# Kernel optimization log

Measured on AMD Instinct MI355X. Metric: run time of the kernel, lower is better.

Reference implementation:

```python
import jax, jax.numpy as jnp
import numpy as np

B, MAXN, D, H, S = 64, 512, 512, 8, 32
DH = D // H          # per-head dim = 64
N = B * MAXN         # 32768 total nodes
E = 524288           # ~avg degree 16
EPS = 1e-5


def setup_inputs() -> dict:
    key = jax.random.key(0)
    ks = jax.random.split(key, 18)
    s = 0.05
    x_dense = jax.random.normal(ks[0], (B, MAXN, D), jnp.float32)
    x = jax.random.normal(ks[1], (N, D), jnp.float32)
    src = jax.random.randint(ks[2], (E,), 0, N)
    # destinations kept within the same graph as the source
    dst = (src // MAXN) * MAXN + jax.random.randint(ks[3], (E,), 0, MAXN)
    edge_index = jnp.stack([src, dst]).astype(jnp.int32)
    batch = (jnp.arange(N) // MAXN).astype(jnp.int32)  # sorted, 512 nodes/graph
    seed = jax.random.normal(ks[4], (S, 1, D), jnp.float32) * s
    # per-head GCN conv weights concatenated along output dim: [D, H*DH] == [D, D]
    Wk = jax.random.normal(ks[5], (D, D), jnp.float32) * s
    bk = jnp.zeros((D,), jnp.float32)
    Wv = jax.random.normal(ks[6], (D, D), jnp.float32) * s
    bv = jnp.zeros((D,), jnp.float32)
    q_proj_weight = jax.random.normal(ks[7], (D, D), jnp.float32) * s
    Wo = jax.random.normal(ks[8], (D, D), jnp.float32) * s
    bo = jnp.zeros((D,), jnp.float32)
    Wff = jax.random.normal(ks[9], (D, D), jnp.float32) * s
    bff = jnp.zeros((D,), jnp.float32)
    gamma_h = jnp.ones((D,), jnp.float32)
    beta_h = jnp.zeros((D,), jnp.float32)
    gamma_z = jnp.ones((D,), jnp.float32)
    beta_z = jnp.zeros((D,), jnp.float32)
    return dict(x_dense=x_dense, x=x, edge_index=edge_index, batch=batch,
                seed=seed, Wk=Wk, bk=bk, Wv=Wv, bv=bv,
                q_proj_weight=q_proj_weight, Wo=Wo, bo=bo, Wff=Wff, bff=bff,
                gamma_h=gamma_h, beta_h=beta_h, gamma_z=gamma_z, beta_z=beta_z)


def _gcn(x, W, b, src, dst):
    # PyG GCNConv with self-loops + symmetric norm; all H heads fused via W [D, H*DH]
    xw = x @ W                                   # [N, D]
    idx = jnp.arange(N)
    src_f = jnp.concatenate([src, idx])
    dst_f = jnp.concatenate([dst, idx])
    deg = jax.ops.segment_sum(jnp.ones_like(dst_f, dtype=x.dtype), dst_f, num_segments=N)
    dinv = jax.lax.rsqrt(deg)                    # deg >= 1 (self-loops)
    norm = dinv[src_f] * dinv[dst_f]             # [E+N]
    out = jax.ops.segment_sum(xw[src_f] * norm[:, None], dst_f, num_segments=N)
    return out + b


def _to_dense(feat, batch):
    # to_dense_batch for sorted batch vector; padded slots are zeros
    counts = jax.ops.segment_sum(jnp.ones((N,), jnp.int32), batch, num_segments=B)
    start = jnp.cumsum(counts) - counts
    pos = jnp.arange(N) - start[batch]
    return jnp.zeros((B, MAXN, feat.shape[-1]), feat.dtype).at[batch, pos].set(feat)


def _layernorm(x, g, b):
    m = jnp.mean(x, -1, keepdims=True)
    v = jnp.mean(jnp.square(x - m), -1, keepdims=True)
    return (x - m) * jax.lax.rsqrt(v + EPS) * g + b


def reference(x_dense, x, edge_index, batch, seed, Wk, bk, Wv, bv,
              q_proj_weight, Wo, bo, Wff, bff, gamma_h, beta_h, gamma_z, beta_z):
    src, dst = edge_index[0], edge_index[1]
    k_nodes = _gcn(x, Wk, bk, src, dst)          # [N, D] (H heads concat)
    v_nodes = _gcn(x, Wv, bv, src, dst)
    k_dense = _to_dense(k_nodes, batch)          # [B, MAXN, D]
    v_dense = _to_dense(v_nodes, batch)

    # query: seed [S,1,D] repeated over batch -> [S,B,D]; q projection (F.linear)
    query = jnp.broadcast_to(seed, (S, B, D))
    q = jnp.einsum('sbd,ed->sbe', query, q_proj_weight)
    scale = 1.0 / jnp.sqrt(jnp.float32(DH))
    qh = (q * scale).reshape(S, B, H, DH).transpose(1, 2, 0, 3)     # [B,H,S,DH]
    kh = k_dense.reshape(B, MAXN, H, DH).transpose(0, 2, 1, 3)      # [B,H,N,DH]
    vh = v_dense.reshape(B, MAXN, H, DH).transpose(0, 2, 1, 3)
    scores = jnp.einsum('bhsd,bhnd->bhsn', qh, kh)                  # [B,H,S,MAXN]
    attn = jax.nn.softmax(scores, axis=-1)                          # no padding mask (faithful)
    ctx = jnp.einsum('bhsn,bhnd->bhsd', attn, vh)                   # [B,H,S,DH]
    ctx = ctx.transpose(0, 2, 1, 3).reshape(B, S, D)                # heads concat
    attn_out = ctx @ Wo.T + bo                                      # [B,S,D]

    query_bse = jnp.broadcast_to(seed.transpose(1, 0, 2), (B, S, D))
    embed = _layernorm(query_bse + attn_out, gamma_h, beta_h)
    embed = _layernorm(embed + embed @ Wff.T + bff, gamma_z, beta_z)
    return embed
```

## Files before the change

### kernel.cpp

```cpp
#include <hip/hip_runtime.h>
#include <hip/hip_bf16.h>

#define BN   64
#define MAXN 512
#define DIM  512
#define NH   8
#define NS   32
#define NN   32768
#define NE   524288
#define NBLK 256
#define EPB  (NE / NBLK)
#define MP   (2048 * 512)

typedef __hip_bfloat16 bf16;
using bf16x8 = __attribute__((ext_vector_type(8))) short;
using f32x4  = __attribute__((ext_vector_type(4))) float;

__device__ int            g_cnt[NN];
__device__ int            g_off[NN + 1];
__device__ int            g_csr[NE];
__device__ unsigned short g_hist[(long)NBLK * NN];
__device__ unsigned short g_bpfx[(long)NBLK * NN];
__device__ float g_dinv[NN];
__device__ bf16  g_xb[NN * DIM];
__device__ bf16  g_agg[NN * DIM];
__device__ bf16  g_aggT[NN * DIM];
__device__ bf16  g_qf[256 * DIM];
__device__ bf16  g_wob[DIM * DIM];
__device__ bf16  g_wvb[DIM * DIM];
__device__ bf16  g_wvo[DIM * 8 * DIM];
__device__ float g_bvo[DIM];
__device__ bf16  g_wffT[DIM * DIM];
__device__ float g_q[NS * DIM];
__device__ bf16  g_sc[BN * 256 * MAXN];
__device__ bf16  g_cp[BN * NS * 8 * DIM];
__device__ float g_part[4 * MP];
__device__ float g_h1[BN * NS * DIM];
__device__ bf16  g_h1b[BN * NS * DIM];

__device__ inline float bf2f(unsigned short u) {
    union { unsigned int i; float f; } x; x.i = ((unsigned int)u) << 16; return x.f;
}

__device__ inline void gll16(const bf16* g, bf16* l) {
    __builtin_amdgcn_global_load_lds(
        (const __attribute__((address_space(1))) void*)g,
        (__attribute__((address_space(3))) void*)l, 16, 0, 0);
}

__global__ __launch_bounds__(512) void k_histprep(const int* __restrict__ dst,
                                                  const float* __restrict__ seed,
                                                  const float* __restrict__ Wq,
                                                  const float* __restrict__ Wo,
                                                  const float* __restrict__ Wv,
                                                  const float* __restrict__ Wff,
                                                  const float* __restrict__ bo,
                                                  const float* __restrict__ bv) {
    __shared__ unsigned int h[NN];
    int blk = blockIdx.x, tid = threadIdx.x;
    if (blk < NBLK) {
        for (int i = tid; i < NN; i += 512) h[i] = 0;
        __syncthreads();
#pragma unroll
        for (int j = 0; j < EPB / 512; j++) {
            int e = blk * EPB + j * 512 + tid;
            atomicAdd(&h[dst[e]], 1u);
        }
        __syncthreads();
        unsigned short* out = g_hist + (long)blk * NN;
        for (int i = tid; i < NN; i += 512) out[i] = (unsigned short)h[i];
    } else if (blk < 288) {
        int i = (blk - 256) * 512 + tid;
        int s = i >> 9, e = i & 511;
        const float* sr = seed + s * DIM;
        const float* wr = Wq + e * DIM;
        float a0 = 0.f, a1 = 0.f;
        for (int d = 0; d < DIM; d += 8) {
            float4 a = *(const float4*)(sr + d);
            float4 b = *(const float4*)(wr + d);
            float4 c = *(const float4*)(sr + d + 4);
            float4 w = *(const float4*)(wr + d + 4);
            a0 += a.x * b.x + a.y * b.y + a.z * b.z + a.w * b.w;
            a1 += c.x * w.x + c.y * w.y + c.z * w.z + c.w * w.w;
        }
        g_q[i] = (a0 + a1) * 0.125f;
    } else if (blk < 480) {
        long t = (long)(blk - 288) * 512 + tid;
        const float* src; bf16* dstp; long off;
        if (t < 32768)      { src = Wo;  dstp = g_wob;  off = t; }
        else if (t < 65536) { src = Wv;  dstp = g_wvb;  off = t - 32768; }
        else                { src = Wff; dstp = g_wffT; off = t - 65536; }
        long i = off * 8;
        float4 a = *(const float4*)(src + i);
        float4 b = *(const float4*)(src + i + 4);
        float v[8] = {a.x, a.y, a.z, a.w, b.x, b.y, b.z, b.w};
        bf16x8 o;
#pragma unroll
        for (int j = 0; j < 8; j++) { bf16 q = __float2bfloat16(v[j]); o[j] = *(short*)&q; }
        *(bf16x8*)(dstp + i) = o;
    } else {
        int e = tid;
        const float* orow = Wo + (long)e * DIM;
        float a0 = 0.f, a1 = 0.f;
        for (int c = 0; c < DIM; c += 8) {
            float4 a = *(const float4*)(bv + c);
            float4 w = *(const float4*)(orow + c);
            float4 xx = *(const float4*)(bv + c + 4);
            float4 u = *(const float4*)(orow + c + 4);
            a0 += a.x * w.x + a.y * w.y + a.z * w.z + a.w * w.w;
            a1 += xx.x * u.x + xx.y * u.y + xx.z * u.z + xx.w * u.w;
        }
        g_bvo[e] = bo[e] + a0 + a1;
    }
}

__global__ __launch_bounds__(256) void k_colscan() {
    int v = blockIdx.x * 256 + threadIdx.x;
    unsigned int s = 0;
#pragma unroll 8
    for (int p = 0; p < NBLK; p++) {
        unsigned int hh = g_hist[(long)p * NN + v];
        g_bpfx[(long)p * NN + v] = (unsigned short)s;
        s += hh;
    }
    g_cnt[v] = (int)s;
    g_dinv[v] = rsqrtf(1.0f + (float)s);
}

__global__ void k_scan() {
    __shared__ int part[1024];
    int t = threadIdx.x;
    int base = t * 32;
    int loc[32]; int s = 0;
#pragma unroll
    for (int i = 0; i < 32; i++) { loc[i] = g_cnt[base + i]; s += loc[i]; }
    part[t] = s; __syncthreads();
    for (int o = 1; o < 1024; o <<= 1) {
        int v = (t >= o) ? part[t - o] : 0;
        __syncthreads();
        part[t] += v;
        __syncthreads();
    }
    int ex = (t == 0) ? 0 : part[t - 1];
#pragma unroll
    for (int i = 0; i < 32; i++) { g_off[base + i] = ex; ex += loc[i]; }
    if (t == 1023) g_off[NN] = ex;
}

__global__ __launch_bounds__(512) void k_fillxb(const int* __restrict__ src,
                                                const int* __restrict__ dst,
                                                const float* __restrict__ x,
                                                const float* __restrict__ Wk) {
    __shared__ unsigned int l[NN];
    int blk = blockIdx.x, tid = threadIdx.x;
    if (blk < NBLK) {
        const unsigned short* bp = g_bpfx + (long)blk * NN;
        for (int i = tid; i < NN; i += 512) l[i] = bp[i];
        __syncthreads();
#pragma unroll
        for (int j = 0; j < EPB / 512; j++) {
            int e = blk * EPB + j * 512 + tid;
            int v = dst[e];
            unsigned int r = atomicAdd(&l[v], 1u);
            g_csr[g_off[v] + r] = src[e];
        }
    } else if (blk < 4352) {
        long i = (long)(blk - 256) * (512 * 8) + (long)tid * 8;
        int node = (int)(i >> 9);
        float w = g_dinv[node];
        float4 a = *(const float4*)(x + i);
        float4 b = *(const float4*)(x + i + 4);
        float v[8] = {a.x, a.y, a.z, a.w, b.x, b.y, b.z, b.w};
        bf16x8 o;
#pragma unroll
        for (int j = 0; j < 8; j++) { bf16 t = __float2bfloat16(v[j] * w); o[j] = *(short*)&t; }
        *(bf16x8*)(g_xb + i) = o;
    } else {
        int i = (blk - 4352) * 512 + tid;
        int hs = i >> 9, d = i & 511;
        int h = hs >> 5, s = hs & 31;
        const float* qr = g_q + s * DIM + h * 64;
        const float* wr = Wk + d * DIM + h * 64;
        float a0 = 0.f, a1 = 0.f;
        for (int t2 = 0; t2 < 64; t2 += 8) {
            float4 a = *(const float4*)(qr + t2);
            float4 w = *(const float4*)(wr + t2);
            float4 c = *(const float4*)(qr + t2 + 4);
            float4 u = *(const float4*)(wr + t2 + 4);
            a0 += a.x * w.x + a.y * w.y + a.z * w.z + a.w * w.w;
            a1 += c.x * u.x + c.y * u.y + c.z * u.z + c.w * u.w;
        }
        g_qf[i] = __float2bfloat16(a0 + a1);
    }
}

__global__ __launch_bounds__(256) void k_gather2() {
    __shared__ float sA[4][576];
    int bid = blockIdx.x;
    int node = (bid & 7) * 4096 + (bid >> 3);
    int w = threadIdx.x >> 6, lane = threadIdx.x & 63;

    float2 acc[4];
#pragma unroll
    for (int j = 0; j < 4; j++) acc[j] = make_float2(0.f, 0.f);

    auto addrow = [&](int s) {
        int4 d = ((const int4*)(g_xb + (long)s * DIM))[lane];
        union { int i; float f; } lo, hi;
#pragma unroll
        for (int j = 0; j < 4; j++) {
            int dw = (j == 0) ? d.x : (j == 1) ? d.y : (j == 2) ? d.z : d.w;
            lo.i = dw << 16;
            hi.i = dw & 0xffff0000;
            acc[j] += make_float2(lo.f, hi.f);
        }
    };

    if (w == 0) addrow(node);
    int e0 = g_off[node], e1 = g_off[node + 1];
    int deg = e1 - e0;
    int m16 = e0 + ((deg >> 4) << 4);
    for (int eb = e0 + w * 4; eb < m16; eb += 16) {
        int s0 = g_csr[eb], s1 = g_csr[eb + 1], s2 = g_csr[eb + 2], s3 = g_csr[eb + 3];
        addrow(s0); addrow(s1); addrow(s2); addrow(s3);
    }
    for (int e = m16 + w; e < e1; e += 4) addrow(g_csr[e]);

#pragma unroll
    for (int j = 0; j < 4; j++) {
        sA[w][lane * 9 + j * 2]     = acc[j].x;
        sA[w][lane * 9 + j * 2 + 1] = acc[j].y;
    }
    __syncthreads();

    int t = threadIdx.x;
    int idx = (t >> 2) * 9 + 2 * (t & 3);
    float s0 = 0.f, s1 = 0.f;
#pragma unroll
    for (int ww = 0; ww < 4; ww++) { s0 += sA[ww][idx]; s1 += sA[ww][idx + 1]; }
    float dd = g_dinv[node];
    bf16 b0 = __float2bfloat16(s0 * dd), b1 = __float2bfloat16(s1 * dd);
    unsigned int word = (unsigned int)*(unsigned short*)&b0 |
                        ((unsigned int)*(unsigned short*)&b1 << 16);
    ((unsigned int*)(g_agg + (long)node * DIM))[t] = word;
}

__device__ __forceinline__ void gemm128(const bf16* __restrict__ A, long lda,
                                        const bf16* __restrict__ Bt, long ldb,
                                        long row0, long col0, int kbeg, int kend,
                                        bf16 (*As)[128 * 32], bf16 (*Bs)[128 * 32],
                                        f32x4 acc[4][4]) {
    int tid = threadIdx.x;
    int lane = tid & 63, wave = tid >> 6;
    int wr = wave >> 1, wc = wave & 1;
    int fr = lane & 15, fq = lane >> 4;
    int rchunk = (fq ^ ((fr >> 1) & 3)) * 8;
    int u0 = wave * 128 + lane;
    int sr0 = u0 >> 2, sc0 = ((u0 & 3) ^ ((sr0 >> 1) & 3)) * 8;
    int u1 = u0 + 64;
    int sr1 = u1 >> 2, sc1 = ((u1 & 3) ^ ((sr1 >> 1) & 3)) * 8;

    auto stage = [&](int buf, int kt) {
        gll16(A + (row0 + sr0) * lda + kt + sc0, As[buf] + u0 * 8);
        gll16(A + (row0 + sr1) * lda + kt + sc1, As[buf] + u1 * 8);
        gll16(Bt + (col0 + sr0) * ldb + kt + sc0, Bs[buf] + u0 * 8);
        gll16(Bt + (col0 + sr1) * ldb + kt + sc1, Bs[buf] + u1 * 8);
    };

    stage(0, kbeg);
    __syncthreads();
    for (int kt = kbeg; kt < kend; kt += 32) {
        int buf = ((kt - kbeg) >> 5) & 1;
        if (kt + 32 < kend) stage(buf ^ 1, kt + 32);
        bf16x8 af[4], bfv[4];
#pragma unroll
        for (int mi = 0; mi < 4; mi++)
            af[mi] = *(const bf16x8*)(As[buf] + (wr * 64 + mi * 16 + fr) * 32 + rchunk);
#pragma unroll
        for (int ni = 0; ni < 4; ni++)
            bfv[ni] = *(const bf16x8*)(Bs[buf] + (wc * 64 + ni * 16 + fr) * 32 + rchunk);
#pragma unroll
        for (int mi = 0; mi < 4; mi++)
#pragma unroll
            for (int ni = 0; ni < 4; ni++)
                acc[mi][ni] = __builtin_amdgcn_mfma_f32_16x16x32_bf16(af[mi], bfv[ni], acc[mi][ni], 0, 0, 0);
        __syncthreads();
    }
}

#define ACC_INIT                                             \
    f32x4 acc[4][4];                                         \
    _Pragma("unroll")                                        \
    for (int i = 0; i < 4; i++)                              \
        _Pragma("unroll")                                    \
        for (int j = 0; j < 4; j++) acc[i][j] = (f32x4){0.f, 0.f, 0.f, 0.f}; \
    int lane = threadIdx.x & 63, wave = threadIdx.x >> 6;    \
    int wr = wave >> 1, wc = wave & 1;                       \
    int fr = lane & 15, fq = lane >> 4;

__global__ __launch_bounds__(256) void k_aggsc() {
    __shared__ __align__(16) char smem[32768];
    int blk = blockIdx.x;
    if (blk < 512) {
        bf16 (*As)[128 * 32] = (bf16(*)[128 * 32])smem;
        bf16 (*Bs)[128 * 32] = (bf16(*)[128 * 32])(smem + 16384);
        int b = blk & 63, bx = (blk >> 6) & 1, by = blk >> 7;
        ACC_INIT
        long row0 = (long)bx * 128, col0 = (long)by * 128;
        gemm128(g_qf, DIM, g_agg + (long)b * (MAXN * DIM), DIM, row0, col0, 0, DIM, As, Bs, acc);
        bf16* out = g_sc + (long)b * (256 * MAXN);
#pragma unroll
        for (int mi = 0; mi < 4; mi++)
#pragma unroll
            for (int ni = 0; ni < 4; ni++) {
                long col = col0 + wc * 64 + ni * 16 + fr;
#pragma unroll
                for (int r = 0; r < 4; r++) {
                    long row = row0 + wr * 64 + mi * 16 + fq * 4 + r;
                    out[row * MAXN + col] = __float2bfloat16(acc[mi][ni][r]);
                }
            }
    } else if (blk < 4608) {
        unsigned short (*L)[72] = (unsigned short(*)[72])smem;
        int id = blk - 512;
        int b = id >> 6, t = id & 63;
        int n0 = (t & 7) * 64, d0 = (t >> 3) * 64;
        int tid = threadIdx.x;
        const unsigned short* src = (const unsigned short*)g_agg + ((long)b * 512 + n0) * 512 + d0;
#pragma unroll
        for (int p = 0; p < 2; p++) {
            int r = (tid >> 3) + 32 * p, c = (tid & 7) * 8;
            *(int4*)&L[r][c] = *(const int4*)(src + (long)r * 512 + c);
        }
        __syncthreads();
        unsigned short* dst = (unsigned short*)g_aggT + ((long)b * 512 + d0) * 512 + n0;
#pragma unroll
        for (int p = 0; p < 2; p++) {
            int dr = (tid >> 3) + 32 * p, c0 = (tid & 7) * 8;
            unsigned short tmp[8];
#pragma unroll
            for (int j = 0; j < 8; j++) tmp[j] = L[c0 + j][dr];
            *(int4*)(dst + (long)dr * 512 + c0) = *(int4*)tmp;
        }
    } else {
        bf16 (*As)[128 * 32] = (bf16(*)[128 * 32])smem;
        bf16 (*Bs)[128 * 32] = (bf16(*)[128 * 32])(smem + 16384);
        int wi = blk - 4608;
        int bx = wi & 3, by = (wi >> 2) & 3, h = wi >> 4;
        ACC_INIT
        long row0 = (long)bx * 128, col0 = (long)by * 128;
        gemm128(g_wob, DIM, g_wvb, DIM, row0, col0, h * 64, h * 64 + 64, As, Bs, acc);
#pragma unroll
        for (int mi = 0; mi < 4; mi++)
#pragma unroll
            for (int ni = 0; ni < 4; ni++) {
                long col = col0 + wc * 64 + ni * 16 + fr;
#pragma unroll
                for (int r = 0; r < 4; r++) {
                    long row = row0 + wr * 64 + mi * 16 + fq * 4 + r;
                    g_wvo[row * 4096 + h * 512 + col] = __float2bfloat16(acc[mi][ni][r]);
                }
            }
    }
}

__global__ __launch_bounds__(256) void k_soft() {
    int w = threadIdx.x >> 6, lane = threadIdx.x & 63;
    unsigned short* base = (unsigned short*)g_sc + ((long)blockIdx.x * 16 + w * 4) * MAXN;
#pragma unroll
    for (int r = 0; r < 4; r++) {
        unsigned short* row = base + (long)r * MAXN;
        float v[8]; float m = -1e30f;
#pragma unroll
        for (int k = 0; k < 8; k++) { v[k] = bf2f(row[lane + 64 * k]); m = fmaxf(m, v[k]); }
#pragma unroll
        for (int o = 32; o > 0; o >>= 1) m = fmaxf(m, __shfl_xor(m, o));
        float sum = 0.f;
#pragma unroll
        for (int k = 0; k < 8; k++) { v[k] = __expf(v[k] - m); sum += v[k]; }
#pragma unroll
        for (int o = 32; o > 0; o >>= 1) sum += __shfl_xor(sum, o);
        float inv = 1.0f / sum;
#pragma unroll
        for (int k = 0; k < 8; k++) {
            bf16 t = __float2bfloat16(v[k] * inv);
            row[lane + 64 * k] = *(unsigned short*)&t;
        }
    }
}

__global__ __launch_bounds__(256) void k_pvg() {
    __shared__ bf16 As[2][128 * 32];
    __shared__ bf16 Bs[2][128 * 32];
    int blk = blockIdx.x;
    int b = blk & 63, bx = (blk >> 6) & 1, by = (blk >> 7) & 1, dh = blk >> 8;
    ACC_INIT
    long row0 = (long)bx * 128, col0 = (long)by * 128;
    gemm128(g_sc + (long)b * (256 * MAXN), MAXN,
            g_aggT + (long)b * (DIM * MAXN) + (long)dh * (256 * MAXN), MAXN,
            row0, col0, 0, MAXN, As, Bs, acc);
#pragma unroll
    for (int mi = 0; mi < 4; mi++)
#pragma unroll
        for (int ni = 0; ni < 4; ni++) {
            long col = col0 + wc * 64 + ni * 16 + fr;
#pragma unroll
            for (int r = 0; r < 4; r++) {
                long row = row0 + wr * 64 + mi * 16 + fq * 4 + r;
                g_cp[((long)b * NS + (row & 31)) * 4096 + (row >> 5) * 512 + dh * 256 + col] =
                    __float2bfloat16(acc[mi][ni][r]);
            }
        }
}

__global__ __launch_bounds__(256) void k_vo() {
    __shared__ bf16 As[2][128 * 32];
    __shared__ bf16 Bs[2][128 * 32];
    ACC_INIT
    int z = blockIdx.z;
    long row0 = (long)blockIdx.x * 128, col0 = (long)blockIdx.y * 128;
    gemm128(g_cp, 4096, g_wvo, 4096, row0, col0, z * 1024, z * 1024 + 1024, As, Bs, acc);
    float* out = g_part + (long)z * MP;
#pragma unroll
    for (int mi = 0; mi < 4; mi++)
#pragma unroll
        for (int ni = 0; ni < 4; ni++) {
            long col = col0 + wc * 64 + ni * 16 + fr;
#pragma unroll
            for (int r = 0; r < 4; r++) {
                long row = row0 + wr * 64 + mi * 16 + fq * 4 + r;
                out[row * DIM + col] = acc[mi][ni][r];
            }
        }
}

__global__ __launch_bounds__(256) void k_ffn() {
    __shared__ bf16 As[2][128 * 32];
    __shared__ bf16 Bs[2][128 * 32];
    ACC_INIT
    int z = blockIdx.z;
    long row0 = (long)blockIdx.x * 128, col0 = (long)blockIdx.y * 128;
    gemm128(g_h1b, DIM, g_wffT, DIM, row0, col0, z * 128, z * 128 + 128, As, Bs, acc);
    float* out = g_part + (long)z * MP;
#pragma unroll
    for (int mi = 0; mi < 4; mi++)
#pragma unroll
        for (int ni = 0; ni < 4; ni++) {
            long col = col0 + wc * 64 + ni * 16 + fr;
#pragma unroll
            for (int r = 0; r < 4; r++) {
                long row = row0 + wr * 64 + mi * 16 + fq * 4 + r;
                out[row * DIM + col] = acc[mi][ni][r];
            }
        }
}

__device__ inline float blockReduceSum(float v, float* red, int tid) {
#pragma unroll
    for (int o = 32; o > 0; o >>= 1) v += __shfl_xor(v, o);
    __syncthreads();
    if ((tid & 63) == 0) red[tid >> 6] = v;
    __syncthreads();
    return red[0] + red[1] + red[2] + red[3];
}

__global__ __launch_bounds__(256) void k_ln1(const float* __restrict__ seed,
                                             const float* __restrict__ gamma,
                                             const float* __restrict__ beta) {
    __shared__ float red[4];
    int r = blockIdx.x, t = threadIdx.x;
    int s = r & 31;
    long base = (long)r * DIM;
    float v0 = seed[s * DIM + t] + g_bvo[t];
    float v1 = seed[s * DIM + 256 + t] + g_bvo[256 + t];
#pragma unroll
    for (int z = 0; z < 4; z++) {
        v0 += g_part[(long)z * MP + base + t];
        v1 += g_part[(long)z * MP + base + 256 + t];
    }
    float mean = blockReduceSum(v0 + v1, red, t) * (1.0f / DIM);
    float d0 = v0 - mean, d1 = v1 - mean;
    float var = blockReduceSum(d0 * d0 + d1 * d1, red, t) * (1.0f / DIM);
    float ri = rsqrtf(var + 1e-5f);
    float o0 = d0 * ri * gamma[t] + beta[t];
    float o1 = d1 * ri * gamma[256 + t] + beta[256 + t];
    g_h1[base + t] = o0; g_h1[base + 256 + t] = o1;
    g_h1b[base + t] = __float2bfloat16(o0);
    g_h1b[base + 256 + t] = __float2bfloat16(o1);
}

__global__ __launch_bounds__(256) void k_ln2(const float* __restrict__ gamma,
                                             const float* __restrict__ beta,
                                             const float* __restrict__ bff,
                                             float* __restrict__ out) {
    __shared__ float red[4];
    int r = blockIdx.x, t = threadIdx.x;
    long base = (long)r * DIM;
    float v0 = g_h1[base + t] + bff[t];
    float v1 = g_h1[base + 256 + t] + bff[256 + t];
#pragma unroll
    for (int z = 0; z < 4; z++) {
        v0 += g_part[(long)z * MP + base + t];
        v1 += g_part[(long)z * MP + base + 256 + t];
    }
    float mean = blockReduceSum(v0 + v1, red, t) * (1.0f / DIM);
    float d0 = v0 - mean, d1 = v1 - mean;
    float var = blockReduceSum(d0 * d0 + d1 * d1, red, t) * (1.0f / DIM);
    float ri = rsqrtf(var + 1e-5f);
    out[base + t] = d0 * ri * gamma[t] + beta[t];
    out[base + 256 + t] = d1 * ri * gamma[256 + t] + beta[256 + t];
}

extern "C" void kernel_launch(void* const* d_in, const int* in_sizes, int n_in,
                              void* d_out, int out_size, void* d_ws, size_t ws_size,
                              hipStream_t stream) {
    (void)in_sizes; (void)n_in; (void)out_size; (void)d_ws; (void)ws_size;
    const float* x    = (const float*)d_in[1];
    const int*   ei   = (const int*)d_in[2];
    const int*   esrc = ei;
    const int*   edst = ei + NE;
    const float* seed = (const float*)d_in[4];
    const float* Wk   = (const float*)d_in[5];
    const float* Wv   = (const float*)d_in[7];
    const float* bv   = (const float*)d_in[8];
    const float* Wq   = (const float*)d_in[9];
    const float* Wo   = (const float*)d_in[10];
    const float* bo   = (const float*)d_in[11];
    const float* Wff  = (const float*)d_in[12];
    const float* bff  = (const float*)d_in[13];
    const float* gh   = (const float*)d_in[14];
    const float* bh   = (const float*)d_in[15];
    const float* gz   = (const float*)d_in[16];
    const float* bz   = (const float*)d_in[17];
    float* out = (float*)d_out;

    k_histprep<<<481, 512, 0, stream>>>(edst, seed, Wq, Wo, Wv, Wff, bo, bv);
    k_colscan <<<NN / 256, 256, 0, stream>>>();
    k_scan    <<<1, 1024, 0, stream>>>();
    k_fillxb  <<<4608, 512, 0, stream>>>(esrc, edst, x, Wk);
    k_gather2 <<<NN, 256, 0, stream>>>();
    k_aggsc   <<<4736, 256, 0, stream>>>();
    k_soft    <<<1024, 256, 0, stream>>>();
    k_pvg     <<<512, 256, 0, stream>>>();
    k_vo      <<<dim3(16, 4, 4), 256, 0, stream>>>();
    k_ln1     <<<BN * NS, 256, 0, stream>>>(seed, gh, bh);
    k_ffn     <<<dim3(16, 4, 4), 256, 0, stream>>>();
    k_ln2     <<<BN * NS, 256, 0, stream>>>(gz, bz, bff, out);
}
```

Baseline: 243.5 us.

## Split fused prep kernels into separate launches and move Wvo GEMM earlier

Breaks the combined histogram+weight-prep kernel and the CSR-fill+x-scale+qf kernel into separate, specialized kernels with 256-thread blocks for the elementwise and prep parts. The Wo·Wv per-head GEMM moves out of k_aggsc into the new k_xbqf launch. The point is to stop heavy 128KB-LDS histogram blocks from sharing a launch with light elementwise blocks, which limits occupancy, and to shorten k_aggsc. In exchange it adds two more kernel launches and removes overlap between independent work.

```diff
diff --git a/kernel.cpp b/kernel.cpp
--- a/kernel.cpp
+++ b/kernel.cpp
@@ -48,29 +48,80 @@
         (__attribute__((address_space(3))) void*)l, 16, 0, 0);
 }
 
-__global__ __launch_bounds__(512) void k_histprep(const int* __restrict__ dst,
-                                                  const float* __restrict__ seed,
-                                                  const float* __restrict__ Wq,
-                                                  const float* __restrict__ Wo,
-                                                  const float* __restrict__ Wv,
-                                                  const float* __restrict__ Wff,
-                                                  const float* __restrict__ bo,
-                                                  const float* __restrict__ bv) {
+__global__ __launch_bounds__(512) void k_hist(const int* __restrict__ dst) {
     __shared__ unsigned int h[NN];
-    int blk = blockIdx.x, tid = threadIdx.x;
-    if (blk < NBLK) {
-        for (int i = tid; i < NN; i += 512) h[i] = 0;
+    int p = blockIdx.x, tid = threadIdx.x;
+    for (int i = tid; i < NN; i += 512) h[i] = 0;
+    __syncthreads();
+#pragma unroll
+    for (int j = 0; j < EPB / 512; j++) {
+        int e = p * EPB + j * 512 + tid;
+        atomicAdd(&h[dst[e]], 1u);
+    }
+    __syncthreads();
+    unsigned short* out = g_hist + (long)p * NN;
+    for (int i = tid; i < NN; i += 512) out[i] = (unsigned short)h[i];
+}
+
+__global__ __launch_bounds__(256) void k_colscan() {
+    int v = blockIdx.x * 256 + threadIdx.x;
+    unsigned int s = 0;
+#pragma unroll 8
+    for (int p = 0; p < NBLK; p++) {
+        unsigned int hh = g_hist[(long)p * NN + v];
+        g_bpfx[(long)p * NN + v] = (unsigned short)s;
+        s += hh;
+    }
+    g_cnt[v] = (int)s;
+    g_dinv[v] = rsqrtf(1.0f + (float)s);
+}
+
+__global__ void k_scan() {
+    __shared__ int part[1024];
+    int t = threadIdx.x;
+    int base = t * 32;
+    int loc[32]; int s = 0;
+#pragma unroll
+    for (int i = 0; i < 32; i++) { loc[i] = g_cnt[base + i]; s += loc[i]; }
+    part[t] = s; __syncthreads();
+    for (int o = 1; o < 1024; o <<= 1) {
+        int v = (t >= o) ? part[t - o] : 0;
         __syncthreads();
-#pragma unroll
-        for (int j = 0; j < EPB / 512; j++) {
-            int e = blk * EPB + j * 512 + tid;
-            atomicAdd(&h[dst[e]], 1u);
-        }
+        part[t] += v;
         __syncthreads();
-        unsigned short* out = g_hist + (long)blk * NN;
-        for (int i = tid; i < NN; i += 512) out[i] = (unsigned short)h[i];
-    } else if (blk < 288) {
-        int i = (blk - 256) * 512 + tid;
+    }
+    int ex = (t == 0) ? 0 : part[t - 1];
+#pragma unroll
+    for (int i = 0; i < 32; i++) { g_off[base + i] = ex; ex += loc[i]; }
+    if (t == 1023) g_off[NN] = ex;
+}
+
+__global__ __launch_bounds__(512) void k_fillsort(const int* __restrict__ src,
+                                                  const int* __restrict__ dst) {
+    __shared__ unsigned int l[NN];
+    int p = blockIdx.x, tid = threadIdx.x;
+    const unsigned short* bp = g_bpfx + (long)p * NN;
+    for (int i = tid; i < NN; i += 512) l[i] = bp[i];
+    __syncthreads();
+#pragma unroll
+    for (int j = 0; j < EPB / 512; j++) {
+        int e = p * EPB + j * 512 + tid;
+        int v = dst[e];
+        unsigned int r = atomicAdd(&l[v], 1u);
+        g_csr[g_off[v] + r] = src[e];
+    }
+}
+
+__global__ __launch_bounds__(256) void k_prep(const float* __restrict__ seed,
+                                              const float* __restrict__ Wq,
+                                              const float* __restrict__ Wo,
+                                              const float* __restrict__ Wv,
+                                              const float* __restrict__ Wff,
+                                              const float* __restrict__ bo,
+                                              const float* __restrict__ bv) {
+    int blk = blockIdx.x;
+    if (blk < 64) {
+        int i = blk * 256 + threadIdx.x;
         int s = i >> 9, e = i & 511;
         const float* sr = seed + s * DIM;
         const float* wr = Wq + e * DIM;
@@ -84,8 +135,8 @@
             a1 += c.x * w.x + c.y * w.y + c.z * w.z + c.w * w.w;
         }
         g_q[i] = (a0 + a1) * 0.125f;
-    } else if (blk < 480) {
-        long t = (long)(blk - 288) * 512 + tid;
+    } else if (blk < 448) {
+        long t = (long)(blk - 64) * 256 + threadIdx.x;
         const float* src; bf16* dstp; long off;
         if (t < 32768)      { src = Wo;  dstp = g_wob;  off = t; }
         else if (t < 65536) { src = Wv;  dstp = g_wvb;  off = t - 32768; }
@@ -99,7 +150,7 @@
         for (int j = 0; j < 8; j++) { bf16 q = __float2bfloat16(v[j]); o[j] = *(short*)&q; }
         *(bf16x8*)(dstp + i) = o;
     } else {
-        int e = tid;
+        int e = (blk - 448) * 256 + threadIdx.x;
         const float* orow = Wo + (long)e * DIM;
         float a0 = 0.f, a1 = 0.f;
         for (int c = 0; c < DIM; c += 8) {
@@ -112,137 +163,6 @@
         }
         g_bvo[e] = bo[e] + a0 + a1;
     }
-}
-
-__global__ __launch_bounds__(256) void k_colscan() {
-    int v = blockIdx.x * 256 + threadIdx.x;
-    unsigned int s = 0;
-#pragma unroll 8
-    for (int p = 0; p < NBLK; p++) {
-        unsigned int hh = g_hist[(long)p * NN + v];
-        g_bpfx[(long)p * NN + v] = (unsigned short)s;
-        s += hh;
-    }
-    g_cnt[v] = (int)s;
-    g_dinv[v] = rsqrtf(1.0f + (float)s);
-}
-
-__global__ void k_scan() {
-    __shared__ int part[1024];
-    int t = threadIdx.x;
-    int base = t * 32;
-    int loc[32]; int s = 0;
-#pragma unroll
-    for (int i = 0; i < 32; i++) { loc[i] = g_cnt[base + i]; s += loc[i]; }
-    part[t] = s; __syncthreads();
-    for (int o = 1; o < 1024; o <<= 1) {
-        int v = (t >= o) ? part[t - o] : 0;
-        __syncthreads();
-        part[t] += v;
-        __syncthreads();
-    }
-    int ex = (t == 0) ? 0 : part[t - 1];
-#pragma unroll
-    for (int i = 0; i < 32; i++) { g_off[base + i] = ex; ex += loc[i]; }
-    if (t == 1023) g_off[NN] = ex;
-}
-
-__global__ __launch_bounds__(512) void k_fillxb(const int* __restrict__ src,
-                                                const int* __restrict__ dst,
-                                                const float* __restrict__ x,
-                                                const float* __restrict__ Wk) {
-    __shared__ unsigned int l[NN];
-    int blk = blockIdx.x, tid = threadIdx.x;
-    if (blk < NBLK) {
-        const unsigned short* bp = g_bpfx + (long)blk * NN;
-        for (int i = tid; i < NN; i += 512) l[i] = bp[i];
-        __syncthreads();
-#pragma unroll
-        for (int j = 0; j < EPB / 512; j++) {
-            int e = blk * EPB + j * 512 + tid;
-            int v = dst[e];
-            unsigned int r = atomicAdd(&l[v], 1u);
-            g_csr[g_off[v] + r] = src[e];
-        }
-    } else if (blk < 4352) {
-        long i = (long)(blk - 256) * (512 * 8) + (long)tid * 8;
-        int node = (int)(i >> 9);
-        float w = g_dinv[node];
-        float4 a = *(const float4*)(x + i);
-        float4 b = *(const float4*)(x + i + 4);
-        float v[8] = {a.x, a.y, a.z, a.w, b.x, b.y, b.z, b.w};
-        bf16x8 o;
-#pragma unroll
-        for (int j = 0; j < 8; j++) { bf16 t = __float2bfloat16(v[j] * w); o[j] = *(short*)&t; }
-        *(bf16x8*)(g_xb + i) = o;
-    } else {
-        int i = (blk - 4352) * 512 + tid;
-        int hs = i >> 9, d = i & 511;
-        int h = hs >> 5, s = hs & 31;
-        const float* qr = g_q + s * DIM + h * 64;
-        const float* wr = Wk + d * DIM + h * 64;
-        float a0 = 0.f, a1 = 0.f;
-        for (int t2 = 0; t2 < 64; t2 += 8) {
-            float4 a = *(const float4*)(qr + t2);
-            float4 w = *(const float4*)(wr + t2);
-            float4 c = *(const float4*)(qr + t2 + 4);
-            float4 u = *(const float4*)(wr + t2 + 4);
-            a0 += a.x * w.x + a.y * w.y + a.z * w.z + a.w * w.w;
-            a1 += c.x * u.x + c.y * u.y + c.z * u.z + c.w * u.w;
-        }
-        g_qf[i] = __float2bfloat16(a0 + a1);
-    }
-}
-
-__global__ __launch_bounds__(256) void k_gather2() {
-    __shared__ float sA[4][576];
-    int bid = blockIdx.x;
-    int node = (bid & 7) * 4096 + (bid >> 3);
-    int w = threadIdx.x >> 6, lane = threadIdx.x & 63;
-
-    float2 acc[4];
-#pragma unroll
-    for (int j = 0; j < 4; j++) acc[j] = make_float2(0.f, 0.f);
-
-    auto addrow = [&](int s) {
-        int4 d = ((const int4*)(g_xb + (long)s * DIM))[lane];
-        union { int i; float f; } lo, hi;
-#pragma unroll
-        for (int j = 0; j < 4; j++) {
-            int dw = (j == 0) ? d.x : (j == 1) ? d.y : (j == 2) ? d.z : d.w;
-            lo.i = dw << 16;
-            hi.i = dw & 0xffff0000;
-            acc[j] += make_float2(lo.f, hi.f);
-        }
-    };
-
-    if (w == 0) addrow(node);
-    int e0 = g_off[node], e1 = g_off[node + 1];
-    int deg = e1 - e0;
-    int m16 = e0 + ((deg >> 4) << 4);
-    for (int eb = e0 + w * 4; eb < m16; eb += 16) {
-        int s0 = g_csr[eb], s1 = g_csr[eb + 1], s2 = g_csr[eb + 2], s3 = g_csr[eb + 3];
-        addrow(s0); addrow(s1); addrow(s2); addrow(s3);
-    }
-    for (int e = m16 + w; e < e1; e += 4) addrow(g_csr[e]);
-
-#pragma unroll
-    for (int j = 0; j < 4; j++) {
-        sA[w][lane * 9 + j * 2]     = acc[j].x;
-        sA[w][lane * 9 + j * 2 + 1] = acc[j].y;
-    }
-    __syncthreads();
-
-    int t = threadIdx.x;
-    int idx = (t >> 2) * 9 + 2 * (t & 3);
-    float s0 = 0.f, s1 = 0.f;
-#pragma unroll
-    for (int ww = 0; ww < 4; ww++) { s0 += sA[ww][idx]; s1 += sA[ww][idx + 1]; }
-    float dd = g_dinv[node];
-    bf16 b0 = __float2bfloat16(s0 * dd), b1 = __float2bfloat16(s1 * dd);
-    unsigned int word = (unsigned int)*(unsigned short*)&b0 |
-                        ((unsigned int)*(unsigned short*)&b1 << 16);
-    ((unsigned int*)(g_agg + (long)node * DIM))[t] = word;
 }
 
 __device__ __forceinline__ void gemm128(const bf16* __restrict__ A, long lda,
@@ -298,6 +218,109 @@
     int wr = wave >> 1, wc = wave & 1;                       \
     int fr = lane & 15, fq = lane >> 4;
 
+__global__ __launch_bounds__(256) void k_xbqf(const float* __restrict__ x,
+                                              const float* __restrict__ Wk) {
+    __shared__ bf16 As[2][128 * 32];
+    __shared__ bf16 Bs[2][128 * 32];
+    int blk = blockIdx.x;
+    if (blk < 8192) {
+        long i = (long)blk * (256 * 8) + (long)threadIdx.x * 8;
+        int node = (int)(i >> 9);
+        float w = g_dinv[node];
+        float4 a = *(const float4*)(x + i);
+        float4 b = *(const float4*)(x + i + 4);
+        float v[8] = {a.x, a.y, a.z, a.w, b.x, b.y, b.z, b.w};
+        bf16x8 o;
+#pragma unroll
+        for (int j = 0; j < 8; j++) { bf16 t = __float2bfloat16(v[j] * w); o[j] = *(short*)&t; }
+        *(bf16x8*)(g_xb + i) = o;
+    } else if (blk < 8704) {
+        int i = (blk - 8192) * 256 + threadIdx.x;
+        int hs = i >> 9, d = i & 511;
+        int h = hs >> 5, s = hs & 31;
+        const float* qr = g_q + s * DIM + h * 64;
+        const float* wr = Wk + d * DIM + h * 64;
+        float a0 = 0.f, a1 = 0.f;
+        for (int t2 = 0; t2 < 64; t2 += 8) {
+            float4 a = *(const float4*)(qr + t2);
+            float4 w = *(const float4*)(wr + t2);
+            float4 c = *(const float4*)(qr + t2 + 4);
+            float4 u = *(const float4*)(wr + t2 + 4);
+            a0 += a.x * w.x + a.y * w.y + a.z * w.z + a.w * w.w;
+            a1 += c.x * u.x + c.y * u.y + c.z * u.z + c.w * u.w;
+        }
+        g_qf[i] = __float2bfloat16(a0 + a1);
+    } else {
+        int wi = blk - 8704;
+        int bx = wi & 3, by = (wi >> 2) & 3, h = wi >> 4;
+        ACC_INIT
+        long row0 = (long)bx * 128, col0 = (long)by * 128;
+        gemm128(g_wob, DIM, g_wvb, DIM, row0, col0, h * 64, h * 64 + 64, As, Bs, acc);
+#pragma unroll
+        for (int mi = 0; mi < 4; mi++)
+#pragma unroll
+            for (int ni = 0; ni < 4; ni++) {
+                long col = col0 + wc * 64 + ni * 16 + fr;
+#pragma unroll
+                for (int r = 0; r < 4; r++) {
+                    long row = row0 + wr * 64 + mi * 16 + fq * 4 + r;
+                    g_wvo[row * 4096 + h * 512 + col] = __float2bfloat16(acc[mi][ni][r]);
+                }
+            }
+    }
+}
+
+__global__ __launch_bounds__(256) void k_gather2() {
+    __shared__ float sA[4][576];
+    int bid = blockIdx.x;
+    int node = (bid & 7) * 4096 + (bid >> 3);
+    int w = threadIdx.x >> 6, lane = threadIdx.x & 63;
+
+    float2 acc[4];
+#pragma unroll
+    for (int j = 0; j < 4; j++) acc[j] = make_float2(0.f, 0.f);
+
+    auto addrow = [&](int s) {
+        int4 d = ((const int4*)(g_xb + (long)s * DIM))[lane];
+        union { int i; float f; } lo, hi;
+#pragma unroll
+        for (int j = 0; j < 4; j++) {
+            int dw = (j == 0) ? d.x : (j == 1) ? d.y : (j == 2) ? d.z : d.w;
+            lo.i = dw << 16;
+            hi.i = dw & 0xffff0000;
+            acc[j] += make_float2(lo.f, hi.f);
+        }
+    };
+
+    if (w == 0) addrow(node);
+    int e0 = g_off[node], e1 = g_off[node + 1];
+    int deg = e1 - e0;
+    int m16 = e0 + ((deg >> 4) << 4);
+    for (int eb = e0 + w * 4; eb < m16; eb += 16) {
+        int s0 = g_csr[eb], s1 = g_csr[eb + 1], s2 = g_csr[eb + 2], s3 = g_csr[eb + 3];
+        addrow(s0); addrow(s1); addrow(s2); addrow(s3);
+    }
+    for (int e = m16 + w; e < e1; e += 4) addrow(g_csr[e]);
+
+#pragma unroll
+    for (int j = 0; j < 4; j++) {
+        sA[w][lane * 9 + j * 2]     = acc[j].x;
+        sA[w][lane * 9 + j * 2 + 1] = acc[j].y;
+    }
+    __syncthreads();
+
+    int t = threadIdx.x;
+    int idx = (t >> 2) * 9 + 2 * (t & 3);
+    float s0 = 0.f, s1 = 0.f;
+#pragma unroll
+    for (int ww = 0; ww < 4; ww++) { s0 += sA[ww][idx]; s1 += sA[ww][idx + 1]; }
+    float dd = g_dinv[node];
+    bf16 b0 = __float2bfloat16(s0 * dd), b1 = __float2bfloat16(s1 * dd);
+    unsigned int word = (unsigned int)*(unsigned short*)&b0 |
+                        ((unsigned int)*(unsigned short*)&b1 << 16);
+    ((unsigned int*)(g_agg + (long)node * DIM))[t] = word;
+}
+
 __global__ __launch_bounds__(256) void k_aggsc() {
     __shared__ __align__(16) char smem[32768];
     int blk = blockIdx.x;
@@ -320,7 +343,7 @@
                     out[row * MAXN + col] = __float2bfloat16(acc[mi][ni][r]);
                 }
             }
-    } else if (blk < 4608) {
+    } else {
         unsigned short (*L)[72] = (unsigned short(*)[72])smem;
         int id = blk - 512;
         int b = id >> 6, t = id & 63;
@@ -342,25 +365,6 @@
             for (int j = 0; j < 8; j++) tmp[j] = L[c0 + j][dr];
             *(int4*)(dst + (long)dr * 512 + c0) = *(int4*)tmp;
         }
-    } else {
-        bf16 (*As)[128 * 32] = (bf16(*)[128 * 32])smem;
-        bf16 (*Bs)[128 * 32] = (bf16(*)[128 * 32])(smem + 16384);
-        int wi = blk - 4608;
-        int bx = wi & 3, by = (wi >> 2) & 3, h = wi >> 4;
-        ACC_INIT
-        long row0 = (long)bx * 128, col0 = (long)by * 128;
-        gemm128(g_wob, DIM, g_wvb, DIM, row0, col0, h * 64, h * 64 + 64, As, Bs, acc);
-#pragma unroll
-        for (int mi = 0; mi < 4; mi++)
-#pragma unroll
-            for (int ni = 0; ni < 4; ni++) {
-                long col = col0 + wc * 64 + ni * 16 + fr;
-#pragma unroll
-                for (int r = 0; r < 4; r++) {
-                    long row = row0 + wr * 64 + mi * 16 + fq * 4 + r;
-                    g_wvo[row * 4096 + h * 512 + col] = __float2bfloat16(acc[mi][ni][r]);
-                }
-            }
     }
 }
 
@@ -534,12 +538,14 @@
     const float* bz   = (const float*)d_in[17];
     float* out = (float*)d_out;
 
-    k_histprep<<<481, 512, 0, stream>>>(edst, seed, Wq, Wo, Wv, Wff, bo, bv);
+    k_hist    <<<NBLK, 512, 0, stream>>>(edst);
     k_colscan <<<NN / 256, 256, 0, stream>>>();
     k_scan    <<<1, 1024, 0, stream>>>();
-    k_fillxb  <<<4608, 512, 0, stream>>>(esrc, edst, x, Wk);
+    k_prep    <<<450, 256, 0, stream>>>(seed, Wq, Wo, Wv, Wff, bo, bv);
+    k_fillsort<<<NBLK, 512, 0, stream>>>(esrc, edst);
+    k_xbqf    <<<8832, 256, 0, stream>>>(x, Wk);
     k_gather2 <<<NN, 256, 0, stream>>>();
-    k_aggsc   <<<4736, 256, 0, stream>>>();
+    k_aggsc   <<<512 + BN * 64, 256, 0, stream>>>();
     k_soft    <<<1024, 256, 0, stream>>>();
     k_pvg     <<<512, 256, 0, stream>>>();
     k_vo      <<<dim3(16, 4, 4), 256, 0, stream>>>();
```

Measured after the change: 231.3 us. -5.0%, faster.
